# Kernel tuning notes

Hardware: AMD Instinct MI355X
Metric: run time of the kernel (lower is better)

Reference implementation:

```python
import jax, jax.numpy as jnp
import numpy as np

B, S, D, H, FF = 2, 2048, 1024, 16, 4096
DK = D // H
LOCAL_WINDOW, STRIDE = 128, 128
NEG = -1000000000.0
EPS = 1e-5


def _layernorm(x, g, b):
    mu = jnp.mean(x, axis=-1, keepdims=True)
    var = jnp.mean(jnp.square(x - mu), axis=-1, keepdims=True)
    return (x - mu) * jax.lax.rsqrt(var + EPS) * g + b


def _strided_mask(seq):
    # allowed(i, j): j <= i and (i-j <= local_window or (i-j) % stride == 0)
    i = jnp.arange(seq)[:, None]
    j = jnp.arange(seq)[None, :]
    d = i - j
    return (d >= 0) & ((d <= LOCAL_WINDOW) | (d % STRIDE == 0))  # [S, S] bool


def setup_inputs() -> dict:
    key = jax.random.key(0)
    ks = jax.random.split(key, 18)
    w = lambda k, shape: jax.random.normal(k, shape, jnp.float32) * 0.02
    return {
        "x": jax.random.normal(ks[0], (B, S, D), jnp.float32),
        "mask": jnp.ones((1, 1, S, S), jnp.int32),
        "Wq": w(ks[1], (D, D)), "bq": jnp.zeros((D,), jnp.float32),
        "Wk": w(ks[2], (D, D)), "bk": jnp.zeros((D,), jnp.float32),
        "Wv": w(ks[3], (D, D)), "bv": jnp.zeros((D,), jnp.float32),
        "Wo": w(ks[4], (D, D)), "bo": jnp.zeros((D,), jnp.float32),
        "W1": w(ks[5], (D, FF)), "bf1": jnp.zeros((FF,), jnp.float32),
        "W2": w(ks[6], (FF, D)), "bf2": jnp.zeros((D,), jnp.float32),
        "g1": jnp.ones((D,), jnp.float32), "bl1": jnp.zeros((D,), jnp.float32),
        "g2": jnp.ones((D,), jnp.float32), "bl2": jnp.zeros((D,), jnp.float32),
    }


def reference(x, mask, Wq, bq, Wk, bk, Wv, bv, Wo, bo,
              W1, bf1, W2, bf2, g1, bl1, g2, bl2):
    b, s, d = x.shape
    sm = _strided_mask(s)[None, None]  # [1,1,S,S]

    # pre-LN self-attention
    n = _layernorm(x, g1, bl1)
    split = lambda t: t.reshape(b, s, H, DK).transpose(0, 2, 1, 3)  # [B,H,S,DK]
    q = split(n @ Wq + bq)
    k = split(n @ Wk + bk)
    v = split(n @ Wv + bv)

    scores = jnp.einsum('bhqd,bhkd->bhqk', q, k) / jnp.sqrt(jnp.float32(DK))
    scores = jnp.where(sm, scores, NEG)          # strided/local mask
    scores = jnp.where(mask == 0, NEG, scores)   # user mask
    attn = jax.nn.softmax(scores, axis=-1)
    o = jnp.einsum('bhqk,bhkd->bhqd', attn, v)
    o = o.transpose(0, 2, 1, 3).reshape(b, s, d) @ Wo + bo
    x = x + o

    # pre-LN FFN (GELU exact, matching torch nn.GELU default)
    n2 = _layernorm(x, g2, bl2)
    ff = jax.nn.gelu(n2 @ W1 + bf1, approximate=False) @ W2 + bf2
    return x + ff
```

## Files before the change

### kernel.cpp

```cpp
#include <hip/hip_runtime.h>
#include <math.h>

typedef unsigned int u32;
typedef unsigned short u16;

#define B_  2
#define S_  2048
#define D_  1024
#define H_  16
#define DK_ 64
#define FF_ 4096
#define NEG_ -1000000000.0f

typedef __attribute__((ext_vector_type(8))) short short8;
typedef __attribute__((ext_vector_type(4))) float floatx4;
typedef __attribute__((ext_vector_type(4))) unsigned short ushort4_t;

__device__ inline u16 f2b(float f) {
    union { float f; u32 u; } v; v.f = f;
    u32 r = (v.u + 0x7fffu + ((v.u >> 16) & 1u)) >> 16;
    return (u16)r;
}
__device__ inline float b2f(u16 b) {
    union { u32 u; float f; } v; v.u = ((u32)b) << 16;
    return v.f;
}

__device__ inline void gl_lds16(const u16* g, u16* l) {
    __builtin_amdgcn_global_load_lds((const __attribute__((address_space(1))) u32*)g,
                                     (__attribute__((address_space(3))) u32*)l, 16, 0, 0);
}

__global__ void tconv4(const float* __restrict__ W0, const float* __restrict__ W1_,
                       const float* __restrict__ W2_, const float* __restrict__ W3,
                       u16* __restrict__ dstBase) {
    __shared__ float tile[32][33];
    int z = blockIdx.z;
    const float* Wm = (z == 0) ? W0 : (z == 1) ? W1_ : (z == 2) ? W2_ : W3;
    u16* Wt = dstBase + (size_t)z * 1024 * 1024;
    const int K = 1024, N = 1024;
    int n0 = blockIdx.x * 32, k0 = blockIdx.y * 32;
    int tx = threadIdx.x & 31, ty = threadIdx.x >> 5;
#pragma unroll
    for (int r = 0; r < 32; r += 8)
        tile[ty + r][tx] = Wm[(size_t)(k0 + ty + r) * N + n0 + tx];
    __syncthreads();
#pragma unroll
    for (int r = 0; r < 32; r += 8)
        Wt[(size_t)(n0 + ty + r) * K + k0 + tx] = f2b(tile[tx][ty + r]);
}

__global__ void tconv(const float* __restrict__ Wm, u16* __restrict__ Wt, int K, int N) {
    __shared__ float tile[32][33];
    int n0 = blockIdx.x * 32, k0 = blockIdx.y * 32;
    int tx = threadIdx.x & 31, ty = threadIdx.x >> 5;
#pragma unroll
    for (int r = 0; r < 32; r += 8)
        tile[ty + r][tx] = Wm[(size_t)(k0 + ty + r) * N + n0 + tx];
    __syncthreads();
#pragma unroll
    for (int r = 0; r < 32; r += 8)
        Wt[(size_t)(n0 + ty + r) * K + k0 + tx] = f2b(tile[tx][ty + r]);
}

__global__ void catbias(const float* __restrict__ bq, const float* __restrict__ bk,
                        const float* __restrict__ bv, float* __restrict__ out) {
    int i = blockIdx.x * 256 + threadIdx.x;
    float v = (i < 1024) ? bq[i] : (i < 2048) ? bk[i - 1024] : bv[i - 2048];
    out[i] = v;
}

__global__ void ln_bf16(const float* __restrict__ x, const float* __restrict__ g,
                        const float* __restrict__ b, u16* __restrict__ out) {
    int row = blockIdx.x;
    int t = threadIdx.x;
    const float* xr = x + (size_t)row * D_;
    __shared__ float red[256];

    float v[4];
    float s = 0.f;
#pragma unroll
    for (int i = 0; i < 4; i++) { v[i] = xr[i * 256 + t]; s += v[i]; }
    red[t] = s; __syncthreads();
    for (int off = 128; off > 0; off >>= 1) {
        if (t < off) red[t] += red[t + off];
        __syncthreads();
    }
    float mu = red[0] * (1.0f / D_);
    __syncthreads();

    float vs = 0.f;
#pragma unroll
    for (int i = 0; i < 4; i++) { float d = v[i] - mu; vs += d * d; }
    red[t] = vs; __syncthreads();
    for (int off = 128; off > 0; off >>= 1) {
        if (t < off) red[t] += red[t + off];
        __syncthreads();
    }
    float rstd = rsqrtf(red[0] * (1.0f / D_) + 1e-5f);

    u16* outr = out + (size_t)row * D_;
#pragma unroll
    for (int i = 0; i < 4; i++) {
        int col = i * 256 + t;
        outr[col] = f2b((v[i] - mu) * rstd * g[col] + b[col]);
    }
}

__global__ __launch_bounds__(256)
void merge_ln(const u16* __restrict__ P, const float* __restrict__ x,
              const float* __restrict__ bo, const float* __restrict__ g,
              const float* __restrict__ bl, float* __restrict__ x1,
              u16* __restrict__ n2) {
    const size_t MN = (size_t)B_ * S_ * D_;
    int row = blockIdx.x, t = threadIdx.x;
    size_t base = (size_t)row * D_;
    __shared__ float red[256];

    float v[4];
    float s = 0.f;
#pragma unroll
    for (int i = 0; i < 4; i++) {
        int col = i * 256 + t;
        float val = x[base + col] + bo[col] + b2f(P[base + col]) + b2f(P[MN + base + col]);
        v[i] = val; s += val;
    }
    red[t] = s; __syncthreads();
    for (int off = 128; off > 0; off >>= 1) {
        if (t < off) red[t] += red[t + off];
        __syncthreads();
    }
    float mu = red[0] * (1.0f / D_);
    __syncthreads();

    float vs = 0.f;
#pragma unroll
    for (int i = 0; i < 4; i++) { float d = v[i] - mu; vs += d * d; }
    red[t] = vs; __syncthreads();
    for (int off = 128; off > 0; off >>= 1) {
        if (t < off) red[t] += red[t + off];
        __syncthreads();
    }
    float rstd = rsqrtf(red[0] * (1.0f / D_) + 1e-5f);

#pragma unroll
    for (int i = 0; i < 4; i++) {
        int col = i * 256 + t;
        x1[base + col] = v[i];
        n2[base + col] = f2b((v[i] - mu) * rstd * g[col] + bl[col]);
    }
}

template <int EPI>
__global__ __launch_bounds__(256, 4)
void gemm_bt(const u16* __restrict__ A, const u16* __restrict__ Bt,
             const float* __restrict__ bias, const float* __restrict__ R,
             void* __restrict__ Cv, int M, int N, int K, int ldA, int ldB) {
    __shared__ u16 As[2][128 * 32];
    __shared__ u16 Bs[2][128 * 32];
    int tid = threadIdx.x;
    int lane = tid & 63, w = tid >> 6;
    int wm = w >> 1, wn = w & 1;
    int m0 = blockIdx.x * 128, n0 = blockIdx.y * 128;
    size_t koff = (size_t)blockIdx.z * K;

    floatx4 acc[4][4];
#pragma unroll
    for (int a = 0; a < 4; a++)
#pragma unroll
        for (int b2 = 0; b2 < 4; b2++) acc[a][b2] = (floatx4){0.f, 0.f, 0.f, 0.f};

    int r4 = lane >> 2;
    int qg = ((lane & 3) ^ ((lane >> 3) & 3)) * 8;
    const u16* Ag0 = A + (size_t)(m0 + w * 16 + r4) * ldA + koff + qg;
    const u16* Bg0 = Bt + (size_t)(n0 + w * 16 + r4) * ldB + koff + qg;
    const int ldsOff = (w * 16) * 32;

    int c = lane & 15, g = lane >> 4;
    int sw = (g ^ ((c >> 1) & 3)) * 8;

    const int nIter = K >> 5;

    gl_lds16(Ag0, &As[0][ldsOff]);
    gl_lds16(Ag0 + (size_t)64 * ldA, &As[0][ldsOff + 64 * 32]);
    gl_lds16(Bg0, &Bs[0][ldsOff]);
    gl_lds16(Bg0 + (size_t)64 * ldB, &Bs[0][ldsOff + 64 * 32]);

    for (int it = 0; it < nIter; it++) {
        __syncthreads();
        int cur = it & 1, nxt = cur ^ 1;
        if (it + 1 < nIter) {
            int kk = (it + 1) << 5;
            gl_lds16(Ag0 + kk, &As[nxt][ldsOff]);
            gl_lds16(Ag0 + kk + (size_t)64 * ldA, &As[nxt][ldsOff + 64 * 32]);
            gl_lds16(Bg0 + kk, &Bs[nxt][ldsOff]);
            gl_lds16(Bg0 + kk + (size_t)64 * ldB, &Bs[nxt][ldsOff + 64 * 32]);
        }
        short8 fa[4], fb[4];
#pragma unroll
        for (int a = 0; a < 4; a++)
            fa[a] = *(const short8*)&As[cur][(wm * 64 + a * 16 + c) * 32 + sw];
#pragma unroll
        for (int b2 = 0; b2 < 4; b2++)
            fb[b2] = *(const short8*)&Bs[cur][(wn * 64 + b2 * 16 + c) * 32 + sw];
#pragma unroll
        for (int a = 0; a < 4; a++)
#pragma unroll
            for (int b2 = 0; b2 < 4; b2++)
                acc[a][b2] = __builtin_amdgcn_mfma_f32_16x16x32_bf16(fa[a], fb[b2], acc[a][b2], 0, 0, 0);
    }

    int mb = m0 + wm * 64, nb = n0 + wn * 64;
#pragma unroll
    for (int a = 0; a < 4; a++) {
#pragma unroll
        for (int b2 = 0; b2 < 4; b2++) {
            int mrow = mb + a * 16 + g * 4;
            int ncol = nb + b2 * 16 + c;
            float bv = (EPI == 3) ? 0.f : bias[ncol];
#pragma unroll
            for (int r = 0; r < 4; r++) {
                int m = mrow + r;
                float vvv = acc[a][b2][r] + bv;
                if (EPI == 0) {
                    int which = ncol >> 10, col = ncol & 1023;
                    int bb = m >> 11, ss = m & 2047, hh = col >> 6, dk = col & 63;
                    ((u16*)Cv)[(size_t)which * ((size_t)B_ * S_ * D_) +
                               ((((size_t)bb * H_ + hh) * S_) + ss) * DK_ + dk] = f2b(vvv);
                } else if (EPI == 1) {
                    ((float*)Cv)[(size_t)m * N + ncol] = vvv + R[(size_t)m * N + ncol];
                } else if (EPI == 2) {
                    float u = 0.79788456080286536f * fmaf(0.044715f * vvv, vvv * vvv, vvv);
                    float th = 1.f - 2.f / (1.f + __expf(2.f * u));
                    ((u16*)Cv)[(size_t)m * N + ncol] = f2b(0.5f * vvv * (1.f + th));
                } else {
                    ((u16*)Cv)[(size_t)blockIdx.z * M * N + (size_t)m * N + ncol] = f2b(vvv);
                }
            }
        }
    }
}

__global__ __launch_bounds__(256)
void ffn2_merge(const u16* __restrict__ P, const float* __restrict__ x1,
                const float* __restrict__ bf2, float* __restrict__ out) {
    const size_t MN = (size_t)B_ * S_ * D_;
    int e = (blockIdx.x * 256 + threadIdx.x) * 4;
    float4 xv = *(const float4*)&x1[e];
    float4 bv = *(const float4*)&bf2[e & 1023];
    float o0 = xv.x + bv.x, o1 = xv.y + bv.y, o2 = xv.z + bv.z, o3 = xv.w + bv.w;
#pragma unroll
    for (int z = 0; z < 4; z++) {
        ushort4_t pv = *(const ushort4_t*)&P[z * MN + e];
        o0 += b2f(pv[0]); o1 += b2f(pv[1]); o2 += b2f(pv[2]); o3 += b2f(pv[3]);
    }
    *(float4*)&out[e] = (float4){o0, o1, o2, o3};
}

__global__ __launch_bounds__(256)
void attn3(const u16* __restrict__ q, const u16* __restrict__ k,
           const u16* __restrict__ v, const int* __restrict__ mask,
           u16* __restrict__ ob) {
    __shared__ u16 Qs[64 * 72];
    __shared__ u16 Kw[192 * 72];
    __shared__ u16 Vt[64 * 200];
    __shared__ u16 Vband[4][16 * 64];
    __shared__ float sb[64][17];

    const int i0 = blockIdx.x * 64;
    const int bh = blockIdx.y;
    const int b  = bh >> 4, h = bh & 15;
    const int t  = threadIdx.x;
    const int lane = t & 63, w = t >> 6;
    const int c = lane & 15, g = lane >> 4;
    const int qloc16 = w * 16;

    const u16* qg = q + ((size_t)bh * S_ + i0) * DK_;
    const u16* kg = k + (size_t)bh * S_ * DK_;
    const u16* vg = v + (size_t)bh * S_ * DK_;

    const int wlo = (i0 >= 128) ? i0 - 128 : 0;
    const int wn  = i0 + 64 - wlo;
    const int nb  = (i0 >= 256) ? (i0 >> 7) - 1 : 0;
    const int jb0 = i0 & 127;
    const int dd0 = i0 - wlo;

    for (int e = t; e < 64 * 8; e += 256) {
        int row = e >> 3, dc = e & 7;
        *(short8*)&Qs[row * 72 + dc * 8] = *(const short8*)(qg + row * 64 + dc * 8);
    }
    for (int e = t; e < wn * 8; e += 256) {
        int row = e >> 3, dc = e & 7;
        *(short8*)&Kw[row * 72 + dc * 8] = *(const short8*)(kg + (size_t)(wlo + row) * 64 + dc * 8);
    }
#pragma unroll
    for (int dc = 0; dc < 8; dc++) {
        for (int jl = t; jl < 192; jl += 256) {
            short8 val = {0, 0, 0, 0, 0, 0, 0, 0};
            if (jl < wn) val = *(const short8*)(vg + (size_t)(wlo + jl) * 64 + dc * 8);
#pragma unroll
            for (int i = 0; i < 8; i++) Vt[(dc * 8 + i) * 200 + jl] = (u16)val[i];
        }
    }
    __syncthreads();

    for (int m = 0; m < nb; m++) {
        int jb = jb0 + (m << 7);
        int jrow = jb + qloc16 + c;
        float p = 0.f;
#pragma unroll
        for (int kc = 0; kc < 2; kc++) {
            short8 kv = *(const short8*)(kg + (size_t)jrow * 64 + kc * 32 + g * 8);
            short8 qv = *(const short8*)&Qs[(qloc16 + c) * 72 + kc * 32 + g * 8];
#pragma unroll
            for (int i = 0; i < 8; i++) p += b2f((u16)qv[i]) * b2f((u16)kv[i]);
        }
        p += __shfl_xor(p, 16);
        p += __shfl_xor(p, 32);
        if (g == 0) {
            int qi = i0 + qloc16 + c;
            float s = p * 0.125f;
            if (mask[(size_t)qi * S_ + jrow] == 0) s = NEG_;
            sb[qloc16 + c][m] = s;
        }
    }

    floatx4 sc[12];
#pragma unroll
    for (int ct = 0; ct < 12; ct++) sc[ct] = (floatx4){0.f, 0.f, 0.f, 0.f};
    short8 fa0 = *(const short8*)&Qs[(qloc16 + c) * 72 + g * 8];
    short8 fa1 = *(const short8*)&Qs[(qloc16 + c) * 72 + 32 + g * 8];
#pragma unroll
    for (int ct = 0; ct < 12; ct++) {
        short8 fb0 = *(const short8*)&Kw[(ct * 16 + c) * 72 + g * 8];
        short8 fb1 = *(const short8*)&Kw[(ct * 16 + c) * 72 + 32 + g * 8];
        sc[ct] = __builtin_amdgcn_mfma_f32_16x16x32_bf16(fa0, fb0, sc[ct], 0, 0, 0);
        sc[ct] = __builtin_amdgcn_mfma_f32_16x16x32_bf16(fa1, fb1, sc[ct], 0, 0, 0);
    }

#pragma unroll
    for (int ct = 0; ct < 12; ct++) {
        int cidx = ct * 16 + c;
        int j = wlo + cidx;
#pragma unroll
        for (int r = 0; r < 4; r++) {
            int qloc = qloc16 + g * 4 + r;
            int d = dd0 + qloc - cidx;
            float s = sc[ct][r] * 0.125f;
            bool ok = false;
            if (d >= 0 && d <= 128) ok = (mask[(size_t)(i0 + qloc) * S_ + j] != 0);
            sc[ct][r] = ok ? s : NEG_;
        }
    }

    float mv[4], inv[4];
#pragma unroll
    for (int r = 0; r < 4; r++) {
        float mm = -1e30f;
#pragma unroll
        for (int ct = 0; ct < 12; ct++) mm = fmaxf(mm, sc[ct][r]);
        mm = fmaxf(mm, __shfl_xor(mm, 1));
        mm = fmaxf(mm, __shfl_xor(mm, 2));
        mm = fmaxf(mm, __shfl_xor(mm, 4));
        mm = fmaxf(mm, __shfl_xor(mm, 8));
        int qloc = qloc16 + g * 4 + r;
        for (int m = 0; m < nb; m++) mm = fmaxf(mm, sb[qloc][m]);
        float sum = 0.f;
#pragma unroll
        for (int ct = 0; ct < 12; ct++) {
            float e = __expf(sc[ct][r] - mm);
            sc[ct][r] = e;
            sum += e;
        }
        sum += __shfl_xor(sum, 1);
        sum += __shfl_xor(sum, 2);
        sum += __shfl_xor(sum, 4);
        sum += __shfl_xor(sum, 8);
        for (int m = 0; m < nb; m++) sum += __expf(sb[qloc][m] - mm);
        mv[r] = mm;
        inv[r] = 1.f / sum;
    }

    __syncthreads();
    u16* P = Kw;
#pragma unroll
    for (int ct = 0; ct < 12; ct++) {
#pragma unroll
        for (int r = 0; r < 4; r++) {
            int qloc = qloc16 + g * 4 + r;
            P[qloc * 200 + ct * 16 + c] = f2b(sc[ct][r]);
        }
    }

    floatx4 o[4];
#pragma unroll
    for (int nt = 0; nt < 4; nt++) o[nt] = (floatx4){0.f, 0.f, 0.f, 0.f};
#pragma unroll
    for (int ks = 0; ks < 6; ks++) {
        short8 pa = *(const short8*)&P[(qloc16 + c) * 200 + ks * 32 + g * 8];
#pragma unroll
        for (int nt = 0; nt < 4; nt++) {
            short8 vb = *(const short8*)&Vt[(nt * 16 + c) * 200 + ks * 32 + g * 8];
            o[nt] = __builtin_amdgcn_mfma_f32_16x16x32_bf16(pa, vb, o[nt], 0, 0, 0);
        }
    }

    for (int m = 0; m < nb; m++) {
        int jb = jb0 + (m << 7);
        asm volatile("s_waitcnt lgkmcnt(0)" ::: "memory");
        __builtin_amdgcn_wave_barrier();
        gl_lds16(vg + (size_t)(jb + qloc16 + (lane >> 3)) * 64 + (lane & 7) * 8, &Vband[w][0]);
        gl_lds16(vg + (size_t)(jb + qloc16 + 8 + (lane >> 3)) * 64 + (lane & 7) * 8, &Vband[w][512]);
        asm volatile("s_waitcnt vmcnt(0)" ::: "memory");
        __builtin_amdgcn_wave_barrier();
#pragma unroll
        for (int r = 0; r < 4; r++) {
            int qloc = qloc16 + g * 4 + r;
            float pb = __expf(sb[qloc][m] - mv[r]);
#pragma unroll
            for (int nt = 0; nt < 4; nt++)
                o[nt][r] += pb * b2f(Vband[w][(g * 4 + r) * 64 + nt * 16 + c]);
        }
    }

#pragma unroll
    for (int nt = 0; nt < 4; nt++) {
#pragma unroll
        for (int r = 0; r < 4; r++) {
            int qi = i0 + qloc16 + g * 4 + r;
            ob[((size_t)b * S_ + qi) * D_ + h * 64 + nt * 16 + c] = f2b(o[nt][r] * inv[r]);
        }
    }
}

extern "C" void kernel_launch(void* const* d_in, const int* in_sizes, int n_in,
                              void* d_out, int out_size, void* d_ws, size_t ws_size,
                              hipStream_t stream) {
    const float* x    = (const float*)d_in[0];
    const int*   mask = (const int*)  d_in[1];
    const float* Wq   = (const float*)d_in[2];
    const float* bq   = (const float*)d_in[3];
    const float* Wk   = (const float*)d_in[4];
    const float* bk   = (const float*)d_in[5];
    const float* Wv   = (const float*)d_in[6];
    const float* bv   = (const float*)d_in[7];
    const float* Wo   = (const float*)d_in[8];
    const float* bo   = (const float*)d_in[9];
    const float* W1   = (const float*)d_in[10];
    const float* bf1  = (const float*)d_in[11];
    const float* W2   = (const float*)d_in[12];
    const float* bf2  = (const float*)d_in[13];
    const float* g1   = (const float*)d_in[14];
    const float* bl1  = (const float*)d_in[15];
    const float* g2   = (const float*)d_in[16];
    const float* bl2  = (const float*)d_in[17];

    char* wsb = (char*)d_ws;
    const size_t MB = 1024 * 1024;
    u16*   WtQKV  = (u16*)(wsb + 0);
    u16*   WtO    = (u16*)(wsb + 6 * MB);
    u16*   Wt1    = (u16*)(wsb + 8 * MB);
    u16*   Wt2    = (u16*)(wsb + 16 * MB);
    u16*   n1b    = (u16*)(wsb + 24 * MB);
    u16*   qkv    = (u16*)(wsb + 32 * MB);
    u16*   obb    = (u16*)(wsb + 56 * MB);
    float* x1     = (float*)(wsb + 32 * MB);
    u16*   ff1b   = (u16*)(wsb + 48 * MB);
    u16*   Ppart  = (u16*)(wsb + 82 * MB);
    u16*   PpartO = (u16*)(wsb + 82 * MB);
    float* bcat   = (float*)(wsb + 114 * MB);
    u16*   n2b    = n1b;

    const int M = B_ * S_;
    const size_t SZ = (size_t)B_ * S_ * D_;

    tconv4<<<dim3(32, 32, 4), 256, 0, stream>>>(Wq, Wk, Wv, Wo, WtQKV);
    tconv<<<dim3(128, 32), 256, 0, stream>>>(W1, Wt1, 1024, 4096);
    tconv<<<dim3(32, 128), 256, 0, stream>>>(W2, Wt2, 4096, 1024);
    catbias<<<12, 256, 0, stream>>>(bq, bk, bv, bcat);

    ln_bf16<<<M, 256, 0, stream>>>(x, g1, bl1, n1b);

    gemm_bt<0><<<dim3(32, 24), 256, 0, stream>>>(n1b, WtQKV, bcat, nullptr, qkv,
                                                 M, 3072, 1024, 1024, 1024);

    attn3<<<dim3(32, 32), 256, 0, stream>>>(qkv, qkv + SZ, qkv + 2 * SZ, mask, obb);

    gemm_bt<3><<<dim3(32, 8, 2), 256, 0, stream>>>(obb, WtO, nullptr, nullptr, PpartO,
                                                   M, 1024, 512, 1024, 1024);
    merge_ln<<<M, 256, 0, stream>>>(PpartO, x, bo, g2, bl2, x1, n2b);

    gemm_bt<2><<<dim3(32, 32), 256, 0, stream>>>(n2b, Wt1, bf1, nullptr, ff1b,
                                                 M, 4096, 1024, 1024, 1024);

    gemm_bt<3><<<dim3(32, 8, 4), 256, 0, stream>>>(ff1b, Wt2, nullptr, nullptr, Ppart,
                                                   M, 1024, 1024, 4096, 4096);
    ffn2_merge<<<(int)(SZ / 1024), 256, 0, stream>>>(Ppart, x1, bf2, (float*)d_out);
}
```

Before: 404.7 us.

## Precompute mask tile flags and restructure attention to skip per-element mask loads

Adds a pre-pass that scans the user mask in 128x128 tiles and records whether each tile is fully unmasked; the attention kernel then skips per-element mask reads when all relevant tiles are set. It also folds the 1/sqrt(dk) scale into the Q projection epilogue, keeps strided-band scores in registers with shuffles instead of shared memory, and loads V for the band directly from global memory instead of through an LDS staging buffer. Shared memory is aliased into one buffer (Q overlaps Vt) to shrink LDS use, moving the V transpose after the softmax. The mask scan adds a full read of the 16 MB mask on every call, which is a new fixed cost.

```diff
diff --git a/kernel.cpp b/kernel.cpp
--- a/kernel.cpp
+++ b/kernel.cpp
@@ -68,6 +68,24 @@
     int i = blockIdx.x * 256 + threadIdx.x;
     float v = (i < 1024) ? bq[i] : (i < 2048) ? bk[i - 1024] : bv[i - 2048];
     out[i] = v;
+}
+
+__global__ __launch_bounds__(256)
+void mask_tiles(const int* __restrict__ mask, int* __restrict__ tflag) {
+    int jt = blockIdx.x, it = blockIdx.y;
+    const int* base = mask + (size_t)it * 128 * S_ + jt * 128;
+    int t = threadIdx.x;
+    int ok = 1;
+    for (int e = t; e < 128 * 32; e += 256) {
+        int r = e >> 5, c4 = e & 31;
+        int4 vv = *(const int4*)&base[(size_t)r * S_ + c4 * 4];
+        ok &= (vv.x != 0) & (vv.y != 0) & (vv.z != 0) & (vv.w != 0);
+    }
+    ok = (int)__all(ok);
+    __shared__ int red[4];
+    if ((t & 63) == 0) red[t >> 6] = ok;
+    __syncthreads();
+    if (t == 0) tflag[it * 16 + jt] = red[0] & red[1] & red[2] & red[3];
 }
 
 __global__ void ln_bf16(const float* __restrict__ x, const float* __restrict__ g,
@@ -224,6 +242,7 @@
                 float vvv = acc[a][b2][r] + bv;
                 if (EPI == 0) {
                     int which = ncol >> 10, col = ncol & 1023;
+                    if (which == 0) vvv *= 0.125f;
                     int bb = m >> 11, ss = m & 2047, hh = col >> 6, dk = col & 63;
                     ((u16*)Cv)[(size_t)which * ((size_t)B_ * S_ * D_) +
                                ((((size_t)bb * H_ + hh) * S_) + ss) * DK_ + dk] = f2b(vvv);
@@ -257,15 +276,15 @@
     *(float4*)&out[e] = (float4){o0, o1, o2, o3};
 }
 
+#define MAXB_ 14
 __global__ __launch_bounds__(256)
-void attn3(const u16* __restrict__ q, const u16* __restrict__ k,
+void attn4(const u16* __restrict__ q, const u16* __restrict__ k,
            const u16* __restrict__ v, const int* __restrict__ mask,
-           u16* __restrict__ ob) {
-    __shared__ u16 Qs[64 * 72];
-    __shared__ u16 Kw[192 * 72];
-    __shared__ u16 Vt[64 * 200];
-    __shared__ u16 Vband[4][16 * 64];
-    __shared__ float sb[64][17];
+           const int* __restrict__ tileOK, u16* __restrict__ ob) {
+    __shared__ u16 sh[26624];
+    u16* Kw = sh;
+    u16* Vt = sh + 13824;
+    u16* Qs = Vt;
 
     const int i0 = blockIdx.x * 64;
     const int bh = blockIdx.y;
@@ -273,6 +292,7 @@
     const int t  = threadIdx.x;
     const int lane = t & 63, w = t >> 6;
     const int c = lane & 15, g = lane >> 4;
+    const int g4 = g * 4;
     const int qloc16 = w * 16;
 
     const u16* qg = q + ((size_t)bh * S_ + i0) * DK_;
@@ -285,6 +305,14 @@
     const int jb0 = i0 & 127;
     const int dd0 = i0 - wlo;
 
+    bool allOK = true;
+    {
+        const int* rowf = tileOK + (i0 >> 7) * 16;
+        int jt0 = wlo >> 7, jt1 = (i0 + 63) >> 7;
+        for (int jt = jt0; jt <= jt1; jt++) allOK &= (rowf[jt] != 0);
+        for (int m = 0; m < nb; m++) allOK &= (rowf[m] != 0);
+    }
+
     for (int e = t; e < 64 * 8; e += 256) {
         int row = e >> 3, dc = e & 7;
         *(short8*)&Qs[row * 72 + dc * 8] = *(const short8*)(qg + row * 64 + dc * 8);
@@ -293,49 +321,46 @@
         int row = e >> 3, dc = e & 7;
         *(short8*)&Kw[row * 72 + dc * 8] = *(const short8*)(kg + (size_t)(wlo + row) * 64 + dc * 8);
     }
-#pragma unroll
-    for (int dc = 0; dc < 8; dc++) {
-        for (int jl = t; jl < 192; jl += 256) {
-            short8 val = {0, 0, 0, 0, 0, 0, 0, 0};
-            if (jl < wn) val = *(const short8*)(vg + (size_t)(wlo + jl) * 64 + dc * 8);
-#pragma unroll
-            for (int i = 0; i < 8; i++) Vt[(dc * 8 + i) * 200 + jl] = (u16)val[i];
-        }
-    }
-    __syncthreads();
-
-    for (int m = 0; m < nb; m++) {
-        int jb = jb0 + (m << 7);
-        int jrow = jb + qloc16 + c;
-        float p = 0.f;
-#pragma unroll
-        for (int kc = 0; kc < 2; kc++) {
-            short8 kv = *(const short8*)(kg + (size_t)jrow * 64 + kc * 32 + g * 8);
-            short8 qv = *(const short8*)&Qs[(qloc16 + c) * 72 + kc * 32 + g * 8];
-#pragma unroll
-            for (int i = 0; i < 8; i++) p += b2f((u16)qv[i]) * b2f((u16)kv[i]);
-        }
-        p += __shfl_xor(p, 16);
-        p += __shfl_xor(p, 32);
-        if (g == 0) {
-            int qi = i0 + qloc16 + c;
-            float s = p * 0.125f;
-            if (mask[(size_t)qi * S_ + jrow] == 0) s = NEG_;
-            sb[qloc16 + c][m] = s;
+    __syncthreads();
+
+    float sbr[MAXB_];
+    {
+        short8 qv0 = *(const short8*)&Qs[(qloc16 + c) * 72 + g * 8];
+        short8 qv1 = *(const short8*)&Qs[(qloc16 + c) * 72 + 32 + g * 8];
+#pragma unroll
+        for (int m = 0; m < MAXB_; m++) {
+            sbr[m] = NEG_;
+            if (m < nb) {
+                int jrow = jb0 + (m << 7) + qloc16 + c;
+                short8 kv0 = *(const short8*)(kg + (size_t)jrow * 64 + g * 8);
+                short8 kv1 = *(const short8*)(kg + (size_t)jrow * 64 + 32 + g * 8);
+                float p = 0.f;
+#pragma unroll
+                for (int i = 0; i < 8; i++) {
+                    p += b2f((u16)qv0[i]) * b2f((u16)kv0[i]);
+                    p += b2f((u16)qv1[i]) * b2f((u16)kv1[i]);
+                }
+                p += __shfl_xor(p, 16);
+                p += __shfl_xor(p, 32);
+                if (!allOK && mask[(size_t)(i0 + qloc16 + c) * S_ + jrow] == 0) p = NEG_;
+                sbr[m] = p;
+            }
         }
     }
 
     floatx4 sc[12];
 #pragma unroll
     for (int ct = 0; ct < 12; ct++) sc[ct] = (floatx4){0.f, 0.f, 0.f, 0.f};
-    short8 fa0 = *(const short8*)&Qs[(qloc16 + c) * 72 + g * 8];
-    short8 fa1 = *(const short8*)&Qs[(qloc16 + c) * 72 + 32 + g * 8];
-#pragma unroll
-    for (int ct = 0; ct < 12; ct++) {
-        short8 fb0 = *(const short8*)&Kw[(ct * 16 + c) * 72 + g * 8];
-        short8 fb1 = *(const short8*)&Kw[(ct * 16 + c) * 72 + 32 + g * 8];
-        sc[ct] = __builtin_amdgcn_mfma_f32_16x16x32_bf16(fa0, fb0, sc[ct], 0, 0, 0);
-        sc[ct] = __builtin_amdgcn_mfma_f32_16x16x32_bf16(fa1, fb1, sc[ct], 0, 0, 0);
+    {
+        short8 fa0 = *(const short8*)&Qs[(qloc16 + c) * 72 + g * 8];
+        short8 fa1 = *(const short8*)&Qs[(qloc16 + c) * 72 + 32 + g * 8];
+#pragma unroll
+        for (int ct = 0; ct < 12; ct++) {
+            short8 fb0 = *(const short8*)&Kw[(ct * 16 + c) * 72 + g * 8];
+            short8 fb1 = *(const short8*)&Kw[(ct * 16 + c) * 72 + 32 + g * 8];
+            sc[ct] = __builtin_amdgcn_mfma_f32_16x16x32_bf16(fa0, fb0, sc[ct], 0, 0, 0);
+            sc[ct] = __builtin_amdgcn_mfma_f32_16x16x32_bf16(fa1, fb1, sc[ct], 0, 0, 0);
+        }
     }
 
 #pragma unroll
@@ -344,18 +369,21 @@
         int j = wlo + cidx;
 #pragma unroll
         for (int r = 0; r < 4; r++) {
-            int qloc = qloc16 + g * 4 + r;
+            int qloc = qloc16 + g4 + r;
             int d = dd0 + qloc - cidx;
-            float s = sc[ct][r] * 0.125f;
-            bool ok = false;
-            if (d >= 0 && d <= 128) ok = (mask[(size_t)(i0 + qloc) * S_ + j] != 0);
-            sc[ct][r] = ok ? s : NEG_;
+            bool ok = (d >= 0) && (d <= 128);
+            if (ok && !allOK) ok = (mask[(size_t)(i0 + qloc) * S_ + j] != 0);
+            sc[ct][r] = ok ? sc[ct][r] : NEG_;
         }
     }
 
     float mv[4], inv[4];
 #pragma unroll
     for (int r = 0; r < 4; r++) {
+        float bs[MAXB_];
+#pragma unroll
+        for (int m = 0; m < MAXB_; m++)
+            bs[m] = (m < nb) ? __shfl(sbr[m], g4 + r, 64) : NEG_;
         float mm = -1e30f;
 #pragma unroll
         for (int ct = 0; ct < 12; ct++) mm = fmaxf(mm, sc[ct][r]);
@@ -363,8 +391,9 @@
         mm = fmaxf(mm, __shfl_xor(mm, 2));
         mm = fmaxf(mm, __shfl_xor(mm, 4));
         mm = fmaxf(mm, __shfl_xor(mm, 8));
-        int qloc = qloc16 + g * 4 + r;
-        for (int m = 0; m < nb; m++) mm = fmaxf(mm, sb[qloc][m]);
+#pragma unroll
+        for (int m = 0; m < MAXB_; m++)
+            if (m < nb) mm = fmaxf(mm, bs[m]);
         float sum = 0.f;
 #pragma unroll
         for (int ct = 0; ct < 12; ct++) {
@@ -376,7 +405,9 @@
         sum += __shfl_xor(sum, 2);
         sum += __shfl_xor(sum, 4);
         sum += __shfl_xor(sum, 8);
-        for (int m = 0; m < nb; m++) sum += __expf(sb[qloc][m] - mm);
+#pragma unroll
+        for (int m = 0; m < MAXB_; m++)
+            if (m < nb) sum += __expf(bs[m] - mm);
         mv[r] = mm;
         inv[r] = 1.f / sum;
     }
@@ -384,13 +415,20 @@
     __syncthreads();
     u16* P = Kw;
 #pragma unroll
-    for (int ct = 0; ct < 12; ct++) {
-#pragma unroll
-        for (int r = 0; r < 4; r++) {
-            int qloc = qloc16 + g * 4 + r;
-            P[qloc * 200 + ct * 16 + c] = f2b(sc[ct][r]);
-        }
-    }
+    for (int ct = 0; ct < 12; ct++)
+#pragma unroll
+        for (int r = 0; r < 4; r++)
+            P[(qloc16 + g4 + r) * 200 + ct * 16 + c] = f2b(sc[ct][r]);
+#pragma unroll
+    for (int dc = 0; dc < 8; dc++) {
+        for (int jl = t; jl < 192; jl += 256) {
+            short8 val = {0, 0, 0, 0, 0, 0, 0, 0};
+            if (jl < wn) val = *(const short8*)(vg + (size_t)(wlo + jl) * 64 + dc * 8);
+#pragma unroll
+            for (int i = 0; i < 8; i++) Vt[(dc * 8 + i) * 200 + jl] = (u16)val[i];
+        }
+    }
+    __syncthreads();
 
     floatx4 o[4];
 #pragma unroll
@@ -405,29 +443,32 @@
         }
     }
 
-    for (int m = 0; m < nb; m++) {
-        int jb = jb0 + (m << 7);
-        asm volatile("s_waitcnt lgkmcnt(0)" ::: "memory");
-        __builtin_amdgcn_wave_barrier();
-        gl_lds16(vg + (size_t)(jb + qloc16 + (lane >> 3)) * 64 + (lane & 7) * 8, &Vband[w][0]);
-        gl_lds16(vg + (size_t)(jb + qloc16 + 8 + (lane >> 3)) * 64 + (lane & 7) * 8, &Vband[w][512]);
-        asm volatile("s_waitcnt vmcnt(0)" ::: "memory");
-        __builtin_amdgcn_wave_barrier();
+#pragma unroll
+    for (int m = 0; m < MAXB_; m++) {
+        if (m < nb) {
+            int vbase = jb0 + (m << 7) + qloc16 + g4;
+            u16 vv[4][4];
+#pragma unroll
+            for (int r = 0; r < 4; r++)
+#pragma unroll
+                for (int nt = 0; nt < 4; nt++)
+                    vv[r][nt] = vg[(size_t)(vbase + r) * 64 + nt * 16 + c];
+#pragma unroll
+            for (int r = 0; r < 4; r++) {
+                float bs = __shfl(sbr[m], g4 + r, 64);
+                float pb = __expf(bs - mv[r]);
+#pragma unroll
+                for (int nt = 0; nt < 4; nt++)
+                    o[nt][r] += pb * b2f(vv[r][nt]);
+            }
+        }
+    }
+
+#pragma unroll
+    for (int nt = 0; nt < 4; nt++) {
 #pragma unroll
         for (int r = 0; r < 4; r++) {
-            int qloc = qloc16 + g * 4 + r;
-            float pb = __expf(sb[qloc][m] - mv[r]);
-#pragma unroll
-            for (int nt = 0; nt < 4; nt++)
-                o[nt][r] += pb * b2f(Vband[w][(g * 4 + r) * 64 + nt * 16 + c]);
-        }
-    }
-
-#pragma unroll
-    for (int nt = 0; nt < 4; nt++) {
-#pragma unroll
-        for (int r = 0; r < 4; r++) {
-            int qi = i0 + qloc16 + g * 4 + r;
+            int qi = i0 + qloc16 + g4 + r;
             ob[((size_t)b * S_ + qi) * D_ + h * 64 + nt * 16 + c] = f2b(o[nt][r] * inv[r]);
         }
     }
@@ -469,11 +510,13 @@
     u16*   Ppart  = (u16*)(wsb + 82 * MB);
     u16*   PpartO = (u16*)(wsb + 82 * MB);
     float* bcat   = (float*)(wsb + 114 * MB);
+    int*   tflag  = (int*)(wsb + 115 * MB);
     u16*   n2b    = n1b;
 
     const int M = B_ * S_;
     const size_t SZ = (size_t)B_ * S_ * D_;
 
+    mask_tiles<<<dim3(16, 16), 256, 0, stream>>>(mask, tflag);
     tconv4<<<dim3(32, 32, 4), 256, 0, stream>>>(Wq, Wk, Wv, Wo, WtQKV);
     tconv<<<dim3(128, 32), 256, 0, stream>>>(W1, Wt1, 1024, 4096);
     tconv<<<dim3(32, 128), 256, 0, stream>>>(W2, Wt2, 4096, 1024);
@@ -484,7 +527,7 @@
     gemm_bt<0><<<dim3(32, 24), 256, 0, stream>>>(n1b, WtQKV, bcat, nullptr, qkv,
                                                  M, 3072, 1024, 1024, 1024);
 
-    attn3<<<dim3(32, 32), 256, 0, stream>>>(qkv, qkv + SZ, qkv + 2 * SZ, mask, obb);
+    attn4<<<dim3(32, 32), 256, 0, stream>>>(qkv, qkv + SZ, qkv + 2 * SZ, mask, tflag, obb);
 
     gemm_bt<3><<<dim3(32, 8, 2), 256, 0, stream>>>(obb, WtO, nullptr, nullptr, PpartO,
                                                    M, 1024, 512, 1024, 1024);
```

Result: faster. 380.7 us (-5.9%).
